# Kernel tuning notes

Hardware: AMD Instinct MI355X
Metric: run time of the kernel (lower is better)

The kernel has to match this reference:

```python
import jax, jax.numpy as jnp
import numpy as np

MAX_SCALE_CAP = 200
STEP = 3


def _shift(a, dy, dx):
    # a[..., y+dy, x+dx] with zero fill outside (dy, dx >= 0), matching the
    # zero-padded dilated 3x3 convs whose only off-center tap is at (+dy,+dx).
    H, W = a.shape[-2], a.shape[-1]
    p = jnp.pad(a, ((0, 0), (0, 0), (0, dy), (0, dx)))
    return p[..., dy:dy + H, dx:dx + W]


def _dif_stacks(Pred, GT, ROI):
    # Builds difPrd / difGT: channel order is (scale major, layer l, direction)
    # directions in dict order: Horizontal (0,+s), Vertical (+s,0), Diagonal (+s,+s)
    B, _, H, W = Pred.shape
    max_scale = min(MAX_SCALE_CAP, max(H, W))
    dP, dG = [], []
    for scale in range(1, max_scale, STEP):
        bP, bG = [], []
        for dy, dx in ((0, scale), (scale, 0), (scale, scale)):
            roi = ROI * _shift(ROI, dy, dx)             # [B,1,H,W]
            bP.append(roi * (Pred - _shift(Pred, dy, dx)))  # [B,3,H,W]
            bG.append(roi * (GT - _shift(GT, dy, dx)))
        # stack dirs on a new axis after layer axis -> l-major, dir-minor
        dP.append(jnp.stack(bP, axis=2).reshape(B, 9, H, W))
        dG.append(jnp.stack(bG, axis=2).reshape(B, 9, H, W))
    return jnp.concatenate(dP, axis=1), jnp.concatenate(dG, axis=1)


def _loss(PredXYZ, GTXYZ, ROIMask):
    difPrd, difGT = _dif_stacks(PredXYZ, GTXYZ, ROIMask)

    # normalization constant per image (detached in the original)
    Rat = jax.nn.relu(difPrd / (difGT + 1e-5))
    absG = jnp.abs(difGT)
    NormConst = (absG * Rat).sum((1, 2, 3)) / ((absG * (Rat > 0)).sum((1, 2, 3)) + 1e-4)
    NormConst = jax.lax.stop_gradient(NormConst)

    c = NormConst                                   # [B]
    safe_c = jnp.where(c > 1e-4, c, 1.0)
    term1 = jnp.where(
        c > 1e-4,
        jnp.abs(difGT - difPrd / safe_c[:, None, None, None]).mean((1, 2, 3)),
        0.0,
    )

    roi_sum = ROIMask.sum((1, 2, 3))
    pos_cnt = (difGT > 0).sum((1, 2, 3)).astype(jnp.float32)
    mean_prd = jnp.abs(difPrd).sum((1, 2, 3)) / pos_cnt

    big = roi_sum > 200
    term2 = jnp.where(big & (mean_prd > 30) & (c > 10), mean_prd - 30.0, 0.0)
    fact = 0.1 / (c + 0.001)
    term3 = jnp.where(big & (mean_prd < 2) & (c < 0.1), (0.2 - mean_prd) * fact, 0.0)

    return (term1 + term2 + term3).sum(), NormConst


def setup_inputs() -> dict:
    key = jax.random.key(0)
    k1, k2, k3 = jax.random.split(key, 3)
    PredXYZ = jax.random.normal(k1, (2, 3, 256, 256), dtype=jnp.float32)
    GTXYZ = jax.random.normal(k2, (2, 3, 256, 256), dtype=jnp.float32)
    ROIMask = (jax.random.uniform(k3, (2, 1, 256, 256)) > 0.3).astype(jnp.float32)
    return {"PredXYZ": PredXYZ, "GTXYZ": GTXYZ, "ROIMask": ROIMask}


def reference(PredXYZ, GTXYZ, ROIMask):
    return _loss(PredXYZ, GTXYZ, ROIMask)
```

## Files before the change

### kernel.cpp

```cpp
#include <hip/hip_runtime.h>


#define NSCALES 67
#define IMG_H 256
#define IMG_W 256
#define NPIX 65536
#define NLINES 2046
#define LMAX_PAD 320


#define ACC_OFF(q, b, s) (32 + (s) * 64 + (q) * 16 + (b) * 8)
#define ROI_OFF(b, s) (544 + (s) * 8 + (b))
#define T1_OFF(b, s) (640 + (s) * 8 + (b))

__device__ __forceinline__ double wave_red(double v) {
#pragma unroll
  for (int o = 32; o > 0; o >>= 1) v += __shfl_down(v, o, 64);
  return v;
}

__device__ __forceinline__ void decode_line(int id, int& b, int& base, int& stride, int& L) {
  if (id < 512) {
    b = id >> 8; int y = id & 255;
    base = y * IMG_W; stride = 1; L = IMG_W;
  } else if (id < 1024) {
    int t = id - 512; b = t >> 8;
    base = t & 255; stride = IMG_W; L = IMG_H;
  } else {
    int t = id - 1024; b = (t >= 511) ? 1 : 0;
    int d = t - b * 511; int c = d - 255;
    int ac = (c < 0) ? -c : c;
    base = (c < 0) ? (-c) * IMG_W : c;
    stride = IMG_W + 1; L = 256 - ac;
  }
}

__device__ __forceinline__ int scale_count(int L, int q) {
  int rem = L - 1 - (q << 6);
  int kcnt = (rem >= 1) ? ((rem - 1) / 3 + 1) : 0;
  return (kcnt > NSCALES) ? NSCALES : kcnt;
}

__device__ __forceinline__ float stage_line(
    const float* __restrict__ Pred, const float* __restrict__ GT,
    const float* __restrict__ ROI, int b, int base, int stride, int L,
    int tid, float4* bufA, float4* bufB) {
  const float* P = Pred + b * (3 * NPIX);
  const float* G = GT + b * (3 * NPIX);
  const float* R = ROI + b * NPIX;
  float r = 0.f, p0 = 0.f, p1 = 0.f, p2 = 0.f, g0 = 0.f, g1 = 0.f, g2 = 0.f;
  if (tid < L) {
    int a = base + tid * stride;
    r = R[a];
    p0 = P[a]; p1 = P[a + NPIX]; p2 = P[a + 2 * NPIX];
    g0 = G[a]; g1 = G[a + NPIX]; g2 = G[a + 2 * NPIX];
  }
  bufA[tid] = make_float4(r, p0, p1, p2);
  bufB[tid] = make_float4(g0, g1, g2, 0.f);
  if (tid < LMAX_PAD - 256) {
    bufA[256 + tid] = make_float4(0.f, 0.f, 0.f, 0.f);
    bufB[256 + tid] = make_float4(0.f, 0.f, 0.f, 0.f);
  }
  __syncthreads();
  return r;
}

extern "C" __global__ void __launch_bounds__(256, 8) pass1_kernel(
    const float* __restrict__ Pred, const float* __restrict__ GT,
    const float* __restrict__ ROI, double* __restrict__ ws) {
  __shared__ float4 bufA[LMAX_PAD];
  __shared__ float4 bufB[LMAX_PAD];
  __shared__ double red[4][5];
  const int id = blockIdx.x;
  const int tid = threadIdx.x;
  const int wid = tid >> 6, lane = tid & 63;

  int b, base, stride, L;
  decode_line(id, b, base, stride, L);
  float stg_r = stage_line(Pred, GT, ROI, b, base, stride, L, tid, bufA, bufB);

  float f1 = 0.f, f2 = 0.f, fp = 0.f;
  int pci = 0;
  int P = 0;
  for (int q = 0; q < 4; ++q) {
    const int Kq = scale_count(L, q);
    int k = (wid - P) & 3;
    if (k < Kq) {
      const int c = (q << 6) + lane;
      const float4 cA = bufA[c];
      const float4 cB = bufB[c];
      const float cr = cA.x, cp0 = cA.y, cp1 = cA.z, cp2 = cA.w;
      const float cg0 = cB.x, cg1 = cB.y, cg2 = cB.z;
      const float4* tA = &bufA[c + 1 + 3 * k];
      const float4* tB = &bufB[c + 1 + 3 * k];
#pragma unroll 2
      for (; k < Kq; k += 4) {
        float4 t0 = tA[0];
        float4 t1 = tB[0];
        tA += 12; tB += 12;
        float rr = cr * t0.x;
#define L1BODY(cp, cg, tp, tg)                                   \
        {                                                        \
          float dP = rr * (cp - tp);                             \
          float dG = rr * (cg - tg);                             \
          float qq = dP * __builtin_amdgcn_rcpf(dG + 1e-5f);     \
          float aG = fabsf(dG);                                  \
          f1 += fmaxf(aG * qq, 0.f);                             \
          if (qq > 0.f) f2 += aG;                                \
          if (dG > 0.f) pci++;                                   \
          fp += fabsf(dP);                                       \
        }
        L1BODY(cp0, cg0, t0.y, t1.x)
        L1BODY(cp1, cg1, t0.z, t1.y)
        L1BODY(cp2, cg2, t0.w, t1.z)
#undef L1BODY
      }
    }
    P += Kq;
  }

  double w0 = wave_red((double)f1);
  double w1 = wave_red((double)f2);
  double w2 = wave_red((double)pci);
  double w3 = wave_red((double)fp);
  double w4 = wave_red((double)stg_r);
  if (lane == 0) {
    red[wid][0] = w0; red[wid][1] = w1; red[wid][2] = w2;
    red[wid][3] = w3; red[wid][4] = w4;
  }
  __syncthreads();
  const int s = id & 7;
  if (tid < 4)
    unsafeAtomicAdd(&ws[ACC_OFF(tid, b, s)],
                    red[0][tid] + red[1][tid] + red[2][tid] + red[3][tid]);
  if (tid == 4 && id < 512)
    unsafeAtomicAdd(&ws[ROI_OFF(b, s)],
                    red[0][4] + red[1][4] + red[2][4] + red[3][4]);
}

extern "C" __global__ void __launch_bounds__(256, 8) pass2_kernel(
    const float* __restrict__ Pred, const float* __restrict__ GT,
    const float* __restrict__ ROI, double* __restrict__ ws) {
  __shared__ float4 bufA[LMAX_PAD];
  __shared__ float4 bufB[LMAX_PAD];
  __shared__ double red[4];
  __shared__ float s_invC[2];
  const int id = blockIdx.x;
  const int tid = threadIdx.x;
  const int wid = tid >> 6, lane = tid & 63;

  int b, base, stride, L;
  decode_line(id, b, base, stride, L);
  if (tid < 2) {
    double S1 = 0.0, S2 = 0.0;
#pragma unroll
    for (int st = 0; st < 8; ++st) {
      S1 += ws[ACC_OFF(0, tid, st)];
      S2 += ws[ACC_OFF(1, tid, st)];
    }
    float cc = (float)(S1 / (S2 + 1e-4));
    s_invC[tid] = (cc > 1e-4f) ? (float)(1.0 / (double)cc) : 1.0f;
  }
  stage_line(Pred, GT, ROI, b, base, stride, L, tid, bufA, bufB);

  const float invC = s_invC[b];
  float f = 0.f;
  int P = 0;
  for (int q = 0; q < 4; ++q) {
    const int Kq = scale_count(L, q);
    int k = (wid - P) & 3;
    if (k < Kq) {
      const int c = (q << 6) + lane;
      const float4 cA = bufA[c];
      const float4 cB = bufB[c];
      const float cr = cA.x, cp0 = cA.y, cp1 = cA.z, cp2 = cA.w;
      const float cg0 = cB.x, cg1 = cB.y, cg2 = cB.z;
      const float4* tA = &bufA[c + 1 + 3 * k];
      const float4* tB = &bufB[c + 1 + 3 * k];
#pragma unroll 2
      for (; k < Kq; k += 4) {
        float4 t0 = tA[0];
        float4 t1 = tB[0];
        tA += 12; tB += 12;
        float rr = cr * t0.x;
        f += rr * fabsf((cg0 - t1.x) - (cp0 - t0.y) * invC);
        f += rr * fabsf((cg1 - t1.y) - (cp1 - t0.z) * invC);
        f += rr * fabsf((cg2 - t1.z) - (cp2 - t0.w) * invC);
      }
    }
    P += Kq;
  }
  double t = wave_red((double)f);
  if (lane == 0) red[wid] = t;
  __syncthreads();
  if (tid == 0)
    unsafeAtomicAdd(&ws[T1_OFF(b, id & 7)],
                    red[0] + red[1] + red[2] + red[3]);
}

extern "C" __global__ void __launch_bounds__(64) final_kernel(
    const double* __restrict__ ws, float* __restrict__ out) {
  if (threadIdx.x == 0) {
    double loss = 0.0;
    for (int b = 0; b < 2; ++b) {
      double S1 = 0.0, S2 = 0.0, PC = 0.0, SP = 0.0, RS = 0.0, T1 = 0.0;
      for (int st = 0; st < 8; ++st) {
        S1 += ws[ACC_OFF(0, b, st)];
        S2 += ws[ACC_OFF(1, b, st)];
        PC += ws[ACC_OFF(2, b, st)];
        SP += ws[ACC_OFF(3, b, st)];
        RS += ws[ROI_OFF(b, st)];
        T1 += ws[T1_OFF(b, st)];
      }
      float cc = (float)(S1 / (S2 + 1e-4));
      out[1 + b] = cc;
      double term1 = (cc > 1e-4f) ? T1 / (603.0 * 65536.0) : 0.0;
      float meanPrd = (float)(SP / PC);
      bool big = RS > 200.0;
      float t2 = (big && meanPrd > 30.f && cc > 10.f) ? (meanPrd - 30.f) : 0.f;
      float fact = 0.1f / (cc + 0.001f);
      float t3 = (big && meanPrd < 2.f && cc < 0.1f) ? (0.2f - meanPrd) * fact : 0.f;
      loss += term1 + (double)(t2 + t3);
    }
    out[0] = (float)loss;
  }
}

extern "C" void kernel_launch(void* const* d_in, const int* in_sizes, int n_in,
                              void* d_out, int out_size, void* d_ws, size_t ws_size,
                              hipStream_t stream) {
  (void)in_sizes; (void)n_in; (void)out_size; (void)ws_size;
  const float* Pred = (const float*)d_in[0];
  const float* GT = (const float*)d_in[1];
  const float* ROI = (const float*)d_in[2];
  float* out = (float*)d_out;
  double* ws = (double*)d_ws;

  hipMemsetAsync(d_ws, 0, 704 * sizeof(double), stream);
  hipLaunchKernelGGL(pass1_kernel, dim3(NLINES), dim3(256), 0, stream,
                     Pred, GT, ROI, ws);
  hipLaunchKernelGGL(pass2_kernel, dim3(NLINES), dim3(256), 0, stream,
                     Pred, GT, ROI, ws);
  hipLaunchKernelGGL(final_kernel, dim3(1), dim3(64), 0, stream, ws, out);
}
```

Baseline: 106.5 us.

## Pack two lines per 512-thread block with 8-wave round-robin scale split

Each block now stages two lines (id and id+1023) into separate shared buffers and runs 8 waves over both lines' scale work. The waves keep a round-robin offset that carries across the two lines, which balances the short diagonal lines against long ones, and the block count is halved. Each block does one reduction covering both lines. In exchange, shared memory and register use per block double, and some waves may idle when the two lines together have few scales.

```diff
diff --git a/kernel.cpp b/kernel.cpp
--- a/kernel.cpp
+++ b/kernel.cpp
@@ -7,6 +7,7 @@
 #define NPIX 65536
 #define NLINES 2046
 #define LMAX_PAD 320
+#define GRID 1023
 
 
 #define ACC_OFF(q, b, s) (32 + (s) * 64 + (q) * 16 + (b) * 8)
@@ -41,116 +42,169 @@
   return (kcnt > NSCALES) ? NSCALES : kcnt;
 }
 
-__device__ __forceinline__ float stage_line(
+__device__ __forceinline__ float stage2(
     const float* __restrict__ Pred, const float* __restrict__ GT,
     const float* __restrict__ ROI, int b, int base, int stride, int L,
-    int tid, float4* bufA, float4* bufB) {
+    int g, int lt, float4 (*bufA)[LMAX_PAD], float4 (*bufB)[LMAX_PAD]) {
   const float* P = Pred + b * (3 * NPIX);
   const float* G = GT + b * (3 * NPIX);
   const float* R = ROI + b * NPIX;
   float r = 0.f, p0 = 0.f, p1 = 0.f, p2 = 0.f, g0 = 0.f, g1 = 0.f, g2 = 0.f;
-  if (tid < L) {
-    int a = base + tid * stride;
+  if (lt < L) {
+    int a = base + lt * stride;
     r = R[a];
     p0 = P[a]; p1 = P[a + NPIX]; p2 = P[a + 2 * NPIX];
     g0 = G[a]; g1 = G[a + NPIX]; g2 = G[a + 2 * NPIX];
   }
-  bufA[tid] = make_float4(r, p0, p1, p2);
-  bufB[tid] = make_float4(g0, g1, g2, 0.f);
-  if (tid < LMAX_PAD - 256) {
-    bufA[256 + tid] = make_float4(0.f, 0.f, 0.f, 0.f);
-    bufB[256 + tid] = make_float4(0.f, 0.f, 0.f, 0.f);
-  }
-  __syncthreads();
+  bufA[g][lt] = make_float4(r, p0, p1, p2);
+  bufB[g][lt] = make_float4(g0, g1, g2, 0.f);
+  if (lt < LMAX_PAD - 256) {
+    bufA[g][256 + lt] = make_float4(0.f, 0.f, 0.f, 0.f);
+    bufB[g][256 + lt] = make_float4(0.f, 0.f, 0.f, 0.f);
+  }
   return r;
 }
 
-extern "C" __global__ void __launch_bounds__(256, 8) pass1_kernel(
+#define L1BODY(cp, cg, tp, tg, F1, F2, PCI, FP)                \
+  {                                                            \
+    float dP = rr * (cp - tp);                                 \
+    float dG = rr * (cg - tg);                                 \
+    float qq = dP * __builtin_amdgcn_rcpf(dG + 1e-5f);         \
+    float aG = fabsf(dG);                                      \
+    F1 += fmaxf(aG * qq, 0.f);                                 \
+    if (qq > 0.f) F2 += aG;                                    \
+    if (dG > 0.f) PCI++;                                       \
+    FP += fabsf(dP);                                           \
+  }
+
+extern "C" __global__ void __launch_bounds__(512, 8) pass1_kernel(
     const float* __restrict__ Pred, const float* __restrict__ GT,
     const float* __restrict__ ROI, double* __restrict__ ws) {
-  __shared__ float4 bufA[LMAX_PAD];
-  __shared__ float4 bufB[LMAX_PAD];
-  __shared__ double red[4][5];
+  __shared__ float4 bufA[2][LMAX_PAD];
+  __shared__ float4 bufB[2][LMAX_PAD];
+  __shared__ double red[8][9];
   const int id = blockIdx.x;
   const int tid = threadIdx.x;
   const int wid = tid >> 6, lane = tid & 63;
-
-  int b, base, stride, L;
-  decode_line(id, b, base, stride, L);
-  float stg_r = stage_line(Pred, GT, ROI, b, base, stride, L, tid, bufA, bufB);
-
-  float f1 = 0.f, f2 = 0.f, fp = 0.f;
-  int pci = 0;
+  const int g = tid >> 8, lt = tid & 255;
+
+  int bA, baseA, strideA, LA;
+  int bB, baseB, strideB, LB;
+  decode_line(id, bA, baseA, strideA, LA);
+  decode_line(id + GRID, bB, baseB, strideB, LB);
+
+  const int myb = g ? bB : bA;
+  const int mybase = g ? baseB : baseA;
+  const int mystride = g ? strideB : strideA;
+  const int myL = g ? LB : LA;
+  float r = stage2(Pred, GT, ROI, myb, mybase, mystride, myL, g, lt, bufA, bufB);
+  float roi_r = (g == 0 && id < 512) ? r : 0.f;
+  __syncthreads();
+
+  float f1 = 0.f, f2 = 0.f, fp = 0.f; int pci = 0;
+  float h1 = 0.f, h2 = 0.f, hp = 0.f; int qci = 0;
   int P = 0;
   for (int q = 0; q < 4; ++q) {
-    const int Kq = scale_count(L, q);
-    int k = (wid - P) & 3;
+    const int Kq = scale_count(LA, q);
+    int k = (wid - P) & 7;
     if (k < Kq) {
       const int c = (q << 6) + lane;
-      const float4 cA = bufA[c];
-      const float4 cB = bufB[c];
+      const float4 cA = bufA[0][c];
+      const float4 cB = bufB[0][c];
       const float cr = cA.x, cp0 = cA.y, cp1 = cA.z, cp2 = cA.w;
       const float cg0 = cB.x, cg1 = cB.y, cg2 = cB.z;
-      const float4* tA = &bufA[c + 1 + 3 * k];
-      const float4* tB = &bufB[c + 1 + 3 * k];
+      const float4* tA = &bufA[0][c + 1 + 3 * k];
+      const float4* tB = &bufB[0][c + 1 + 3 * k];
 #pragma unroll 2
-      for (; k < Kq; k += 4) {
+      for (; k < Kq; k += 8) {
         float4 t0 = tA[0];
         float4 t1 = tB[0];
-        tA += 12; tB += 12;
+        tA += 24; tB += 24;
         float rr = cr * t0.x;
-#define L1BODY(cp, cg, tp, tg)                                   \
-        {                                                        \
-          float dP = rr * (cp - tp);                             \
-          float dG = rr * (cg - tg);                             \
-          float qq = dP * __builtin_amdgcn_rcpf(dG + 1e-5f);     \
-          float aG = fabsf(dG);                                  \
-          f1 += fmaxf(aG * qq, 0.f);                             \
-          if (qq > 0.f) f2 += aG;                                \
-          if (dG > 0.f) pci++;                                   \
-          fp += fabsf(dP);                                       \
-        }
-        L1BODY(cp0, cg0, t0.y, t1.x)
-        L1BODY(cp1, cg1, t0.z, t1.y)
-        L1BODY(cp2, cg2, t0.w, t1.z)
-#undef L1BODY
+        L1BODY(cp0, cg0, t0.y, t1.x, f1, f2, pci, fp)
+        L1BODY(cp1, cg1, t0.z, t1.y, f1, f2, pci, fp)
+        L1BODY(cp2, cg2, t0.w, t1.z, f1, f2, pci, fp)
       }
     }
     P += Kq;
   }
-
-  double w0 = wave_red((double)f1);
-  double w1 = wave_red((double)f2);
-  double w2 = wave_red((double)pci);
-  double w3 = wave_red((double)fp);
-  double w4 = wave_red((double)stg_r);
+  for (int q = 0; q < 4; ++q) {
+    const int Kq = scale_count(LB, q);
+    int k = (wid - P) & 7;
+    if (k < Kq) {
+      const int c = (q << 6) + lane;
+      const float4 cA = bufA[1][c];
+      const float4 cB = bufB[1][c];
+      const float cr = cA.x, cp0 = cA.y, cp1 = cA.z, cp2 = cA.w;
+      const float cg0 = cB.x, cg1 = cB.y, cg2 = cB.z;
+      const float4* tA = &bufA[1][c + 1 + 3 * k];
+      const float4* tB = &bufB[1][c + 1 + 3 * k];
+#pragma unroll 2
+      for (; k < Kq; k += 8) {
+        float4 t0 = tA[0];
+        float4 t1 = tB[0];
+        tA += 24; tB += 24;
+        float rr = cr * t0.x;
+        L1BODY(cp0, cg0, t0.y, t1.x, h1, h2, qci, hp)
+        L1BODY(cp1, cg1, t0.z, t1.y, h1, h2, qci, hp)
+        L1BODY(cp2, cg2, t0.w, t1.z, h1, h2, qci, hp)
+      }
+    }
+    P += Kq;
+  }
+
+  double vA0 = wave_red((double)f1);
+  double vA1 = wave_red((double)f2);
+  double vA2 = wave_red((double)pci);
+  double vA3 = wave_red((double)fp);
+  double vA4 = wave_red((double)roi_r);
+  double vB0 = wave_red((double)h1);
+  double vB1 = wave_red((double)h2);
+  double vB2 = wave_red((double)qci);
+  double vB3 = wave_red((double)hp);
   if (lane == 0) {
-    red[wid][0] = w0; red[wid][1] = w1; red[wid][2] = w2;
-    red[wid][3] = w3; red[wid][4] = w4;
+    red[wid][0] = vA0; red[wid][1] = vA1; red[wid][2] = vA2;
+    red[wid][3] = vA3; red[wid][4] = vA4;
+    red[wid][5] = vB0; red[wid][6] = vB1; red[wid][7] = vB2;
+    red[wid][8] = vB3;
   }
   __syncthreads();
   const int s = id & 7;
-  if (tid < 4)
-    unsafeAtomicAdd(&ws[ACC_OFF(tid, b, s)],
-                    red[0][tid] + red[1][tid] + red[2][tid] + red[3][tid]);
-  if (tid == 4 && id < 512)
-    unsafeAtomicAdd(&ws[ROI_OFF(b, s)],
-                    red[0][4] + red[1][4] + red[2][4] + red[3][4]);
-}
-
-extern "C" __global__ void __launch_bounds__(256, 8) pass2_kernel(
+  if (tid < 4) {
+    double v = 0.0;
+#pragma unroll
+    for (int w = 0; w < 8; ++w) v += red[w][tid];
+    unsafeAtomicAdd(&ws[ACC_OFF(tid, bA, s)], v);
+  } else if (tid >= 8 && tid < 12) {
+    const int q = tid - 8;
+    double v = 0.0;
+#pragma unroll
+    for (int w = 0; w < 8; ++w) v += red[w][5 + q];
+    unsafeAtomicAdd(&ws[ACC_OFF(q, bB, s)], v);
+  }
+  if (tid == 16 && id < 512) {
+    double v = red[0][4] + red[1][4] + red[2][4] + red[3][4];
+    unsafeAtomicAdd(&ws[ROI_OFF(bA, s)], v);
+  }
+}
+
+extern "C" __global__ void __launch_bounds__(512, 8) pass2_kernel(
     const float* __restrict__ Pred, const float* __restrict__ GT,
     const float* __restrict__ ROI, double* __restrict__ ws) {
-  __shared__ float4 bufA[LMAX_PAD];
-  __shared__ float4 bufB[LMAX_PAD];
-  __shared__ double red[4];
+  __shared__ float4 bufA[2][LMAX_PAD];
+  __shared__ float4 bufB[2][LMAX_PAD];
+  __shared__ double red[8][2];
   __shared__ float s_invC[2];
   const int id = blockIdx.x;
   const int tid = threadIdx.x;
   const int wid = tid >> 6, lane = tid & 63;
-
-  int b, base, stride, L;
-  decode_line(id, b, base, stride, L);
+  const int g = tid >> 8, lt = tid & 255;
+
+  int bA, baseA, strideA, LA;
+  int bB, baseB, strideB, LB;
+  decode_line(id, bA, baseA, strideA, LA);
+  decode_line(id + GRID, bB, baseB, strideB, LB);
+
   if (tid < 2) {
     double S1 = 0.0, S2 = 0.0;
 #pragma unroll
@@ -161,41 +215,75 @@
     float cc = (float)(S1 / (S2 + 1e-4));
     s_invC[tid] = (cc > 1e-4f) ? (float)(1.0 / (double)cc) : 1.0f;
   }
-  stage_line(Pred, GT, ROI, b, base, stride, L, tid, bufA, bufB);
-
-  const float invC = s_invC[b];
-  float f = 0.f;
+  const int myb = g ? bB : bA;
+  const int mybase = g ? baseB : baseA;
+  const int mystride = g ? strideB : strideA;
+  const int myL = g ? LB : LA;
+  stage2(Pred, GT, ROI, myb, mybase, mystride, myL, g, lt, bufA, bufB);
+  __syncthreads();
+
+  const float invCA = s_invC[bA];
+  const float invCB = s_invC[bB];
+  float fA = 0.f, fB = 0.f;
   int P = 0;
   for (int q = 0; q < 4; ++q) {
-    const int Kq = scale_count(L, q);
-    int k = (wid - P) & 3;
+    const int Kq = scale_count(LA, q);
+    int k = (wid - P) & 7;
     if (k < Kq) {
       const int c = (q << 6) + lane;
-      const float4 cA = bufA[c];
-      const float4 cB = bufB[c];
+      const float4 cA = bufA[0][c];
+      const float4 cB = bufB[0][c];
       const float cr = cA.x, cp0 = cA.y, cp1 = cA.z, cp2 = cA.w;
       const float cg0 = cB.x, cg1 = cB.y, cg2 = cB.z;
-      const float4* tA = &bufA[c + 1 + 3 * k];
-      const float4* tB = &bufB[c + 1 + 3 * k];
+      const float4* tA = &bufA[0][c + 1 + 3 * k];
+      const float4* tB = &bufB[0][c + 1 + 3 * k];
 #pragma unroll 2
-      for (; k < Kq; k += 4) {
+      for (; k < Kq; k += 8) {
         float4 t0 = tA[0];
         float4 t1 = tB[0];
-        tA += 12; tB += 12;
+        tA += 24; tB += 24;
         float rr = cr * t0.x;
-        f += rr * fabsf((cg0 - t1.x) - (cp0 - t0.y) * invC);
-        f += rr * fabsf((cg1 - t1.y) - (cp1 - t0.z) * invC);
-        f += rr * fabsf((cg2 - t1.z) - (cp2 - t0.w) * invC);
+        fA += rr * fabsf((cg0 - t1.x) - (cp0 - t0.y) * invCA);
+        fA += rr * fabsf((cg1 - t1.y) - (cp1 - t0.z) * invCA);
+        fA += rr * fabsf((cg2 - t1.z) - (cp2 - t0.w) * invCA);
       }
     }
     P += Kq;
   }
-  double t = wave_red((double)f);
-  if (lane == 0) red[wid] = t;
+  for (int q = 0; q < 4; ++q) {
+    const int Kq = scale_count(LB, q);
+    int k = (wid - P) & 7;
+    if (k < Kq) {
+      const int c = (q << 6) + lane;
+      const float4 cA = bufA[1][c];
+      const float4 cB = bufB[1][c];
+      const float cr = cA.x, cp0 = cA.y, cp1 = cA.z, cp2 = cA.w;
+      const float cg0 = cB.x, cg1 = cB.y, cg2 = cB.z;
+      const float4* tA = &bufA[1][c + 1 + 3 * k];
+      const float4* tB = &bufB[1][c + 1 + 3 * k];
+#pragma unroll 2
+      for (; k < Kq; k += 8) {
+        float4 t0 = tA[0];
+        float4 t1 = tB[0];
+        tA += 24; tB += 24;
+        float rr = cr * t0.x;
+        fB += rr * fabsf((cg0 - t1.x) - (cp0 - t0.y) * invCB);
+        fB += rr * fabsf((cg1 - t1.y) - (cp1 - t0.z) * invCB);
+        fB += rr * fabsf((cg2 - t1.z) - (cp2 - t0.w) * invCB);
+      }
+    }
+    P += Kq;
+  }
+  double tA_ = wave_red((double)fA);
+  double tB_ = wave_red((double)fB);
+  if (lane == 0) { red[wid][0] = tA_; red[wid][1] = tB_; }
   __syncthreads();
-  if (tid == 0)
-    unsafeAtomicAdd(&ws[T1_OFF(b, id & 7)],
-                    red[0] + red[1] + red[2] + red[3]);
+  if (tid < 2) {
+    double v = 0.0;
+#pragma unroll
+    for (int w = 0; w < 8; ++w) v += red[w][tid];
+    unsafeAtomicAdd(&ws[T1_OFF(tid == 0 ? bA : bB, id & 7)], v);
+  }
 }
 
 extern "C" __global__ void __launch_bounds__(64) final_kernel(
@@ -237,9 +325,9 @@
   double* ws = (double*)d_ws;
 
   hipMemsetAsync(d_ws, 0, 704 * sizeof(double), stream);
-  hipLaunchKernelGGL(pass1_kernel, dim3(NLINES), dim3(256), 0, stream,
+  hipLaunchKernelGGL(pass1_kernel, dim3(GRID), dim3(512), 0, stream,
                      Pred, GT, ROI, ws);
-  hipLaunchKernelGGL(pass2_kernel, dim3(NLINES), dim3(256), 0, stream,
+  hipLaunchKernelGGL(pass2_kernel, dim3(GRID), dim3(512), 0, stream,
                      Pred, GT, ROI, ws);
   hipLaunchKernelGGL(final_kernel, dim3(1), dim3(64), 0, stream, ws, out);
 }
```

New measurement: 118.3 us. +11.1%, slower.
